# Performance work log

Measured on AMD Instinct MI355X. Metric: run time of the kernel, lower is better.

## Reference

```python
import jax, jax.numpy as jnp
import numpy as np

B, C, H, L, P = 2048, 128, 4, 2, 106
D = C // H
N_PRED = B * P


def _ln(x, g, b, eps=1e-5):
    m = jnp.mean(x, -1, keepdims=True)
    v = jnp.mean((x - m) ** 2, -1, keepdims=True)
    return (x - m) / jnp.sqrt(v + eps) * g + b


def _seg_softmax(a, seg, n):
    mx = jax.lax.stop_gradient(jax.ops.segment_max(a, seg, num_segments=n))
    e = jnp.exp(a - mx[seg])
    den = jax.ops.segment_sum(e, seg, num_segments=n)
    return e / jnp.maximum(den[seg], 1e-16)


def _hgt_layer(xn, xp, edges, kqv_nw, kqv_nb, kqv_pw, kqv_pb, a_rel, m_rel, p_rel,
               out_nw, out_nb, out_pw, out_pb, skip_n, skip_p):
    # PyG HGTConv: per-node-type KQV, per-edge-type relation transforms, grouped
    # softmax over all incoming edges per destination node, scatter-sum aggregation.
    e_np_src, e_np_dst, e_pn_src, e_pn_dst = edges
    nn_, np_ = xn.shape[0], xp.shape[0]
    kqv_n = (xn @ kqv_nw + kqv_nb).reshape(nn_, 3, H, D)
    kqv_p = (xp @ kqv_pw + kqv_pb).reshape(np_, 3, H, D)
    kn, qn, vn = kqv_n[:, 0], kqv_n[:, 1], kqv_n[:, 2]
    kp, qp, vp = kqv_p[:, 0], kqv_p[:, 1], kqv_p[:, 2]
    # relation-specific (per edge type, per head) transforms of all source nodes
    k0 = jnp.einsum('nhd,hde->nhe', kn, a_rel[0])  # news -> predicate
    v0 = jnp.einsum('nhd,hde->nhe', vn, m_rel[0])
    k1 = jnp.einsum('nhd,hde->nhe', kp, a_rel[1])  # predicate -> news
    v1 = jnp.einsum('nhd,hde->nhe', vp, m_rel[1])
    scale = 1.0 / jnp.sqrt(jnp.float32(D))
    a0 = jnp.sum(qp[e_np_dst] * k0[e_np_src], -1) * p_rel[0] * scale  # [E0,H]
    a1 = jnp.sum(qn[e_pn_dst] * k1[e_pn_src], -1) * p_rel[1] * scale  # [E1,H]
    n_tot = nn_ + np_
    dst = jnp.concatenate([e_np_dst + nn_, e_pn_dst])  # global dst ids (news first)
    alpha = _seg_softmax(jnp.concatenate([a0, a1]), dst, n_tot)
    msg = jnp.concatenate([v0[e_np_src], v1[e_pn_src]])  # [E,H,D]
    agg = jax.ops.segment_sum(alpha[..., None] * msg, dst, num_segments=n_tot)
    agg = agg.reshape(n_tot, H * D)
    on = jax.nn.gelu(agg[:nn_], approximate=False) @ out_nw + out_nb
    op = jax.nn.gelu(agg[nn_:], approximate=False) @ out_pw + out_pb
    sn = jax.nn.sigmoid(skip_n)
    sp = jax.nn.sigmoid(skip_p)
    return sn * on + (1.0 - sn) * xn, sp * op + (1.0 - sp) * xp


def setup_inputs():
    ks = iter(jax.random.split(jax.random.key(0), 64))
    rn = lambda shape, s=0.02: jax.random.normal(next(ks), shape, jnp.float32) * s
    i = {}
    i['news_emb'] = jax.random.normal(next(ks), (B, 1024), jnp.float32)
    i['base_embs'] = jax.random.normal(next(ks), (P, 1024), jnp.float32)
    i['ctx_w'] = rn((1024, C)); i['ctx_b'] = jnp.zeros((C,), jnp.float32)
    i['proj_w'] = rn((1024, C)); i['proj_b'] = jnp.zeros((C,), jnp.float32)
    i['fus_w'] = rn((2 * C, C)); i['fus_b'] = jnp.zeros((C,), jnp.float32)
    i['enc_w'] = rn((1024, C)); i['enc_b'] = jnp.zeros((C,), jnp.float32)
    i['enc_g'] = jnp.ones((C,), jnp.float32); i['enc_beta'] = jnp.zeros((C,), jnp.float32)
    for t in ('n', 'p'):
        i['lin_%sw' % t] = rn((C, C)); i['lin_%sb' % t] = jnp.zeros((C,), jnp.float32)
        i['lin_%sg' % t] = jnp.ones((C,), jnp.float32); i['lin_%sbeta' % t] = jnp.zeros((C,), jnp.float32)
        i['kqv_%sw' % t] = rn((L, C, 3 * C)); i['kqv_%sb' % t] = jnp.zeros((L, 3 * C), jnp.float32)
        i['out_%sw' % t] = rn((L, C, C)); i['out_%sb' % t] = jnp.zeros((L, C), jnp.float32)
        i['skip_%s' % t] = jnp.ones((L,), jnp.float32)
        i['ln_%sg' % t] = jnp.ones((L, C), jnp.float32); i['ln_%sbeta' % t] = jnp.zeros((L, C), jnp.float32)
    i['a_rel'] = rn((L, 2, H, D, D), 0.1)
    i['m_rel'] = rn((L, 2, H, D, D), 0.1)
    i['p_rel'] = jnp.ones((L, 2, H), jnp.float32)
    i['cls_w'] = rn((C, 2)); i['cls_b'] = jnp.zeros((2,), jnp.float32)
    # news node b owns predicate nodes [b*P, (b+1)*P)
    i['e_np_src'] = jnp.repeat(jnp.arange(B), P)
    i['e_np_dst'] = jnp.arange(N_PRED)
    i['e_pn_src'] = jnp.arange(N_PRED)
    i['e_pn_dst'] = jnp.repeat(jnp.arange(B), P)
    return i


def reference(news_emb, base_embs, ctx_w, ctx_b, proj_w, proj_b, fus_w, fus_b,
              enc_w, enc_b, enc_g, enc_beta,
              lin_nw, lin_nb, lin_ng, lin_nbeta, lin_pw, lin_pb, lin_pg, lin_pbeta,
              kqv_nw, kqv_nb, kqv_pw, kqv_pb, out_nw, out_nb, out_pw, out_pb,
              skip_n, skip_p, ln_ng, ln_nbeta, ln_pg, ln_pbeta,
              a_rel, m_rel, p_rel, cls_w, cls_b,
              e_np_src, e_np_dst, e_pn_src, e_pn_dst):
    b = news_emb.shape[0]
    # DynamicEmbedding: context-conditioned predicate embeddings [b, P, C]
    news_ctx = news_emb @ ctx_w + ctx_b
    pred_base = base_embs @ proj_w + proj_b
    fused = jnp.concatenate([jnp.broadcast_to(pred_base[None], (b, P, C)),
                             jnp.broadcast_to(news_ctx[:, None], (b, P, C))], -1)
    xp = (fused @ fus_w + fus_b).reshape(b * P, C)
    # news encoder: Linear -> LayerNorm -> ELU
    xn = jax.nn.elu(_ln(news_emb @ enc_w + enc_b, enc_g, enc_beta))
    res_n, res_p = xn, xp
    xn = _ln(xn @ lin_nw + lin_nb, lin_ng, lin_nbeta) + res_n
    xp = _ln(xp @ lin_pw + lin_pb, lin_pg, lin_pbeta) + res_p
    edges = (e_np_src, e_np_dst, e_pn_src, e_pn_dst)
    for l in range(L):
        xn2, xp2 = _hgt_layer(xn, xp, edges, kqv_nw[l], kqv_nb[l], kqv_pw[l], kqv_pb[l],
                              a_rel[l], m_rel[l], p_rel[l],
                              out_nw[l], out_nb[l], out_pw[l], out_pb[l],
                              skip_n[l], skip_p[l])
        xn = jax.nn.elu(_ln(xn2 + res_n, ln_ng[l], ln_nbeta[l]))
        xp = jax.nn.elu(_ln(xp2 + res_p, ln_pg[l], ln_pbeta[l]))
        res_n, res_p = xn, xp
    logits = xn @ cls_w + cls_b
    # attention output is constant by construction in the original module:
    # uniform 1/107 everywhere, row (news -> predicates) overwritten with
    # mean of the dummy uniform per-edge weights = 1/num_edges.
    e0 = e_np_src.shape[0]
    att = jnp.full((b, P + 1, P + 1, H), 1.0 / (P + 1), jnp.float32)
    att = att.at[:, 0, 1:, :].set(1.0 / e0)
    return logits, att
```

## Files before the change

kernel.cpp:

```cpp
#include <hip/hip_runtime.h>
#include <math.h>


#define DEVFN __device__ __forceinline__

typedef float nfloat4 __attribute__((ext_vector_type(4)));

DEVFN void nt_store4(float4* addr, float v){
  nfloat4 val = {v,v,v,v};
  __builtin_nontemporal_store(val, reinterpret_cast<nfloat4*>(addr));
}

DEVFN float wsum(float v){
#pragma unroll
  for (int o=32;o;o>>=1) v += __shfl_xor(v,o);
  return v;
}
DEVFN float wmaxr(float v){
#pragma unroll
  for (int o=32;o;o>>=1) v = fmaxf(v,__shfl_xor(v,o));
  return v;
}
DEVFN float gelu_f(float x){ return 0.5f*x*(1.f+erff(x*0.70710678118654752f)); }
DEVFN float elu_f(float x){ return x>0.f?x:expm1f(x); }
DEVFN float sigm(float x){ return 1.f/(1.f+expf(-x)); }

__global__ __launch_bounds__(512,2) void mega(
  const float* __restrict__ xn_enc_g, const float* __restrict__ Vv_g,
  const float* __restrict__ B1v_g, const float* __restrict__ sb1_g,
  const float* __restrict__ AU, const float* __restrict__ AUT,
  const float* __restrict__ sa1,
  const float* __restrict__ Wcomb, const float* __restrict__ bcomb,
  const float* __restrict__ WvC, const float* __restrict__ bv2,
  const float* __restrict__ Wnv, const float* __restrict__ bnv,
  const float* __restrict__ lin_nw, const float* __restrict__ lin_nb,
  const float* __restrict__ lin_ng, const float* __restrict__ lin_nbeta,
  const float* __restrict__ lin_pg, const float* __restrict__ lin_pbeta,
  const float* __restrict__ ln_pg, const float* __restrict__ ln_pbeta,
  const float* __restrict__ out_nw, const float* __restrict__ out_nb,
  const float* __restrict__ out_pw, const float* __restrict__ out_pb,
  const float* __restrict__ skip_n, const float* __restrict__ skip_p,
  const float* __restrict__ ln_ng, const float* __restrict__ ln_nbeta,
  const float* __restrict__ cls_w, const float* __restrict__ cls_b,
  float* __restrict__ out)
{
  __shared__ __align__(16) float xe[512], x1[512], xA[512], W0s[512], Bv[512], Vvs[512];
  __shared__ __align__(16) float scratch[2048];
  __shared__ __align__(16) float ss[2048];
  __shared__ __align__(16) float rowa[512], rowb[512];
  __shared__ float inv0[512], m1s[512], i1s[512];
  __shared__ __align__(16) float4 PK0[256];
  __shared__ __align__(16) float2 PE[256];
  __shared__ __align__(16) float2 Fa[256];
  __shared__ __align__(16) float4 G0B0[64];
  __shared__ __align__(16) float x4T[512];
  const int tid=threadIdx.x, lane=tid&63, wave=tid>>6, w2=wave>>1, half=wave&1;
  const int bid = blockIdx.x;
  const bool isfill = ((bid%3)==2) && (bid/3 < 253);
  if (isfill){
    float4* att4 = reinterpret_cast<float4*>(out + 4096);
    const long b0 = 24 + (long)(bid/3)*8;
#pragma unroll
    for (int r=0;r<8;r++){
      long base=(b0+r)*11449L;
      for (int i=tid;i<11449;i+=512){
        float v=(i>=1&&i<107)?(1.f/217088.f):(1.f/107.f);
        nt_store4(&att4[base+i], v);
      }
    }
    return;
  }
  int nf = (bid+1)/3; if (nf>253) nf=253;
  const int cid = bid - nf;
  const int bbase=cid*4, b=bbase+w2;
  const float sp0=sigm(skip_p[0]), omsp=1.f-sp0, c1=1.f+omsp;
  xe[tid]=xn_enc_g[(long)bbase*128+tid];
  Bv[tid]=B1v_g[(long)bbase*128+tid];
  Vvs[tid]=Vv_g[(long)bbase*128+tid];
  if (tid<64) G0B0[tid]=make_float4(ln_pg[2*tid],ln_pg[2*tid+1],ln_pbeta[2*tid],ln_pbeta[2*tid+1]);
  __syncthreads();
  if (tid<256){
    int wp=tid>>6, c=tid&63;
    float bx=Bv[wp*128+2*c], by=Bv[wp*128+2*c+1];
    PK0[tid]=make_float4(bx,by,lin_pg[2*c],lin_pg[2*c+1]);
    PE[tid]=make_float2(lin_pbeta[2*c]+Vvs[wp*128+2*c], lin_pbeta[2*c+1]+Vvs[wp*128+2*c+1]);
  }
  {
    const int r=tid>>7, j=tid&127;
    const float4* x4=(const float4*)(xe+r*128);
    float a0=lin_nb[j],a1=0.f,a2=0.f,a3=0.f;
#pragma unroll 4
    for (int i=0;i<32;i++){
      float4 xv=x4[i]; int k=4*i;
      a0+=xv.x*lin_nw[k*128+j]; a1+=xv.y*lin_nw[(k+1)*128+j];
      a2+=xv.z*lin_nw[(k+2)*128+j]; a3+=xv.w*lin_nw[(k+3)*128+j];
    }
    rowa[tid]=(a0+a1)+(a2+a3);
  }
  __syncthreads();
  const float4* AU4=(const float4*)AU;
  const float4* AUT4=(const float4*)AUT;
  const float sb = sb1_g[b];
  const int p = half*64 + lane;
  const bool act = (p<106);
  float iv_reg=0.f;
  if (act){
    float dt0=0.f, dt1=0.f;
#pragma unroll 4
    for (int c=0;c<64;c++){
      float4 au=AUT4[c*128+p];
      float4 pk=PK0[w2*64+c];
      dt0 += au.x*pk.x; dt1 += au.y*pk.y;
    }
    iv_reg = rsqrtf((sa1[p]+2.f*(dt0+dt1)+sb)*(1.f/128.f)+1e-5f);
    inv0[w2*128+p]=iv_reg;
  }
  if (half==0){
    const float* rw=rowa+w2*128;
    float t0=rw[lane], t1=rw[lane+64];
    float m=wsum(t0+t1)*(1.f/128.f);
    float d0=t0-m,d1=t1-m;
    float var=wsum(d0*d0+d1*d1)*(1.f/128.f);
    float inv=rsqrtf(var+1e-5f);
    float v0=d0*inv*lin_ng[lane]   +lin_nbeta[lane]   +xe[w2*128+lane];
    float v1=d1*inv*lin_ng[lane+64]+lin_nbeta[lane+64]+xe[w2*128+lane+64];
    x1[w2*128+lane]=v0; x1[w2*128+lane+64]=v1;
    x4T[lane*4+w2]=v0; x4T[(lane+64)*4+w2]=v1;
  }
  __syncthreads();
  {
    float bval=bcomb[tid];
    float p0=bval,p1=bval,p2=bval,p3=bval, q0=0.f,q1=0.f,q2=0.f,q3=0.f;
    const float4* xv4=(const float4*)x4T;
#pragma unroll 4
    for (int k=0;k<128;k+=2){
      float4 xv=xv4[k];  float w=Wcomb[k*512+tid];
      p0+=xv.x*w; p1+=xv.y*w; p2+=xv.z*w; p3+=xv.w*w;
      float4 xv2=xv4[k+1]; float w2=Wcomb[(k+1)*512+tid];
      q0+=xv2.x*w2; q1+=xv2.y*w2; q2+=xv2.z*w2; q3+=xv2.w*w2;
    }
    int h=tid>>7, cc=tid&127, c=cc>>1, par=cc&1;
    int base = c*8 + (h>>1)*4 + (h&1)*2 + par;
    scratch[base]=p0+q0; scratch[512+base]=p1+q1; scratch[1024+base]=p2+q2; scratch[1536+base]=p3+q3;
  }
  __syncthreads();
  if (act){
    const float iv=iv_reg;
    const float4* qp=(const float4*)(scratch+w2*512);
    float s0=0,s1=0,s2=0,s3=0, u0=0,u1=0,u2=0,u3=0;
#pragma unroll 2
    for (int c=0;c<64;c+=2){
      {
        float4 au=AUT4[c*128+p];
        float4 pk=PK0[w2*64+c];
        float2 e=PE[w2*64+c];
        float4 Qa=qp[c*2], Qb=qp[c*2+1];
        float rx=(au.x+pk.x)*iv*pk.z + e.x + au.z;
        float ry=(au.y+pk.y)*iv*pk.w + e.y + au.w;
        s0+=rx*Qa.x+ry*Qa.y; s1+=rx*Qa.z+ry*Qa.w;
        s2+=rx*Qb.x+ry*Qb.y; s3+=rx*Qb.z+ry*Qb.w;
      }
      {
        int c2=c+1;
        float4 au=AUT4[c2*128+p];
        float4 pk=PK0[w2*64+c2];
        float2 e=PE[w2*64+c2];
        float4 Qa=qp[c2*2], Qb=qp[c2*2+1];
        float rx=(au.x+pk.x)*iv*pk.z + e.x + au.z;
        float ry=(au.y+pk.y)*iv*pk.w + e.y + au.w;
        u0+=rx*Qa.x+ry*Qa.y; u1+=rx*Qa.z+ry*Qa.w;
        u2+=rx*Qb.x+ry*Qb.y; u3+=rx*Qb.z+ry*Qb.w;
      }
    }
    ss[w2*512+  0+p]=s0+u0; ss[w2*512+128+p]=s1+u1;
    ss[w2*512+256+p]=s2+u2; ss[w2*512+384+p]=s3+u3;
  }
  __syncthreads();
#pragma unroll
  for (int k=0;k<2;k++){
    int jj=wave*2+k, jb=jj>>2, jh=jj&3;
    float* row = ss + jb*512 + jh*128;
    float v1=(lane<106)? row[lane] : -1e30f;
    float v2=(lane+64<106)? row[lane+64] : -1e30f;
    float mx=wmaxr(fmaxf(v1,v2));
    float e1=(lane<106)? expf(v1-mx):0.f;
    float e2=(lane+64<106)? expf(v2-mx):0.f;
    float den=wsum(e1+e2);
    float rinv=1.f/den;
    if (lane<106) row[lane]=e1*rinv;
    if (lane+64<106) row[lane+64]=e2*rinv;
  }
  __syncthreads();
  float2 yb0,yb1,yb2,yb3;
  {
    float4 pk=PK0[w2*64+lane];
    float2 e=PE[w2*64+lane];
    float2 y0={0,0},y1={0,0},y2={0,0},y3={0,0};
    const float* al = ss + w2*512;
    const float* ivp = inv0 + w2*128;
    const int pst=half*53, pen=pst+53;
    for (int pp=pst; pp<pen; pp++){
      float4 au=AU4[pp*64+lane];
      float ivv=ivp[pp];
      float rx=(au.x+pk.x)*ivv*pk.z+e.x+au.z;
      float ry=(au.y+pk.y)*ivv*pk.w+e.y+au.w;
      float a0=al[pp],a1=al[128+pp],a2=al[256+pp],a3=al[384+pp];
      y0.x+=a0*rx; y0.y+=a0*ry; y1.x+=a1*rx; y1.y+=a1*ry;
      y2.x+=a2*rx; y2.y+=a2*ry; y3.x+=a3*rx; y3.y+=a3*ry;
    }
    yb0=y0; yb1=y1; yb2=y2; yb3=y3;
    if (half==0){
      float2* Yw=(float2*)(scratch+w2*512);
      Yw[lane]=y0; Yw[64+lane]=y1; Yw[128+lane]=y2; Yw[192+lane]=y3;
    }
  }
  __syncthreads();
  if (half==1){
    float2* Yw=(float2*)(scratch+w2*512);
    float2 t;
    t=Yw[lane];     t.x+=yb0.x; t.y+=yb0.y; Yw[lane]=t;
    t=Yw[64+lane];  t.x+=yb1.x; t.y+=yb1.y; Yw[64+lane]=t;
    t=Yw[128+lane]; t.x+=yb2.x; t.y+=yb2.y; Yw[128+lane]=t;
    t=Yw[192+lane]; t.x+=yb3.x; t.y+=yb3.y; Yw[192+lane]=t;
  }
  __syncthreads();
  float* rowd = ss + 512;
  {
    const int r=tid>>7, j=tid&127, h=j>>5, d=j&31;
    const float4* y4=(const float4*)(scratch + r*512 + h*128);
    const float4* x4=(const float4*)(x1 + r*128);
    const float* Wp = WvC + (h*128)*32 + d;
    float a1a=bv2[j], a1b=0.f, a2a=bnv[j], a2b=0.f;
#pragma unroll 2
    for (int i=0;i<32;i+=2){
      float4 yv=y4[i]; float4 xv=x4[i]; int cc=4*i;
      a1a += yv.x*Wp[cc*32]+yv.y*Wp[(cc+1)*32]+yv.z*Wp[(cc+2)*32]+yv.w*Wp[(cc+3)*32];
      a2a += xv.x*Wnv[cc*128+j]+xv.y*Wnv[(cc+1)*128+j]+xv.z*Wnv[(cc+2)*128+j]+xv.w*Wnv[(cc+3)*128+j];
      float4 yv2=y4[i+1]; float4 xv2=x4[i+1]; int c2=4*i+4;
      a1b += yv2.x*Wp[c2*32]+yv2.y*Wp[(c2+1)*32]+yv2.z*Wp[(c2+2)*32]+yv2.w*Wp[(c2+3)*32];
      a2b += xv2.x*Wnv[c2*128+j]+xv2.y*Wnv[(c2+1)*128+j]+xv2.z*Wnv[(c2+2)*128+j]+xv2.w*Wnv[(c2+3)*128+j];
    }
    rowb[tid]=gelu_f(a1a+a1b); rowd[tid]=gelu_f(a2a+a2b);
  }
  __syncthreads();
  {
    const int r=tid>>7, j=tid&127;
    const float4* xb=(const float4*)(rowb+r*128);
    const float4* xd=(const float4*)(rowd+r*128);
    float a1a=out_nb[j], a1b=0.f, a2a=out_pb[j], a2b=0.f;
#pragma unroll 2
    for (int i=0;i<32;i+=2){
      float4 bv_=xb[i]; float4 dv=xd[i]; int cc=4*i;
      a1a += bv_.x*out_nw[cc*128+j]+bv_.y*out_nw[(cc+1)*128+j]+bv_.z*out_nw[(cc+2)*128+j]+bv_.w*out_nw[(cc+3)*128+j];
      a2a += dv.x*out_pw[cc*128+j]+dv.y*out_pw[(cc+1)*128+j]+dv.z*out_pw[(cc+2)*128+j]+dv.w*out_pw[(cc+3)*128+j];
      float4 bv2_=xb[i+1]; float4 dv2=xd[i+1]; int c2=4*i+4;
      a1b += bv2_.x*out_nw[c2*128+j]+bv2_.y*out_nw[(c2+1)*128+j]+bv2_.z*out_nw[(c2+2)*128+j]+bv2_.w*out_nw[(c2+3)*128+j];
      a2b += dv2.x*out_pw[c2*128+j]+dv2.y*out_pw[(c2+1)*128+j]+dv2.z*out_pw[(c2+2)*128+j]+dv2.w*out_pw[(c2+3)*128+j];
    }
    rowa[tid]=a1a+a1b; W0s[tid]=a2a+a2b;
  }
  __syncthreads();
  if (half==0){
    float sn=sigm(skip_n[0]), os=1.f-sn;
    const float* A=rowa+w2*128; const float* Bx=x1+w2*128; const float* R=xe+w2*128;
    float t0=sn*A[lane]+os*Bx[lane]+R[lane];
    float t1=sn*A[lane+64]+os*Bx[lane+64]+R[lane+64];
    float m=wsum(t0+t1)*(1.f/128.f);
    float d0=t0-m,d1=t1-m;
    float var=wsum(d0*d0+d1*d1)*(1.f/128.f);
    float inv=rsqrtf(var+1e-5f);
    float v0=elu_f(d0*inv*ln_ng[lane]+ln_nbeta[lane]);
    float v1=elu_f(d1*inv*ln_ng[lane+64]+ln_nbeta[lane+64]);
    xA[w2*128+lane]=v0; xA[w2*128+lane+64]=v1;
    x4T[lane*4+w2]=v0; x4T[(lane+64)*4+w2]=v1;
  }
  if (tid<256){
    int wp=tid>>6, c=tid&63;
    Fa[tid]=make_float2(omsp*PE[tid].x + sp0*W0s[wp*128+2*c]   + Vvs[wp*128+2*c],
                        omsp*PE[tid].y + sp0*W0s[wp*128+2*c+1] + Vvs[wp*128+2*c+1]);
  }
  __syncthreads();
  {
    float bval=bcomb[512+tid];
    float p0=bval,p1=bval,p2=bval,p3=bval, q0=0.f,q1=0.f,q2=0.f,q3=0.f;
    const float4* xv4=(const float4*)x4T;
    const float* W=Wcomb+65536;
#pragma unroll 4
    for (int k=0;k<128;k+=2){
      float4 xv=xv4[k];  float w=W[k*512+tid];
      p0+=xv.x*w; p1+=xv.y*w; p2+=xv.z*w; p3+=xv.w*w;
      float4 xv2=xv4[k+1]; float w2=W[(k+1)*512+tid];
      q0+=xv2.x*w2; q1+=xv2.y*w2; q2+=xv2.z*w2; q3+=xv2.w*w2;
    }
    int h=tid>>7, cc=tid&127, c=cc>>1, par=cc&1;
    int base = c*8 + (h>>1)*4 + (h&1)*2 + par;
    scratch[base]=p0+q0; scratch[512+base]=p1+q1; scratch[1024+base]=p2+q2; scratch[1536+base]=p3+q3;
  }
  __syncthreads();
  if (act){
    const float iv=iv_reg;
    float st0=0.f, st1=0.f, sq0=0.f, sq1=0.f;
#pragma unroll 2
    for (int c=0;c<64;c+=2){
      {
        float4 au=AUT4[c*128+p];
        float4 pk=PK0[w2*64+c];
        float2 f=Fa[w2*64+c];
        float t0=omsp*((au.x+pk.x)*iv*pk.z) + f.x + c1*au.z;
        float t1=omsp*((au.y+pk.y)*iv*pk.w) + f.y + c1*au.w;
        st0+=t0+t1; sq0+=t0*t0+t1*t1;
      }
      {
        int c2=c+1;
        float4 au=AUT4[c2*128+p];
        float4 pk=PK0[w2*64+c2];
        float2 f=Fa[w2*64+c2];
        float t0=omsp*((au.x+pk.x)*iv*pk.z) + f.x + c1*au.z;
        float t1=omsp*((au.y+pk.y)*iv*pk.w) + f.y + c1*au.w;
        st1+=t0+t1; sq1+=t0*t0+t1*t1;
      }
    }
    float mA=(st0+st1)*(1.f/128.f);
    float ivA=rsqrtf(fmaxf((sq0+sq1)*(1.f/128.f)-mA*mA,0.f)+1e-5f);
    m1s[w2*128+p]=mA; i1s[w2*128+p]=ivA;
    const float4* qp=(const float4*)(scratch+w2*512);
    float s0=0,s1=0,s2=0,s3=0, u0=0,u1=0,u2=0,u3=0;
#pragma unroll 2
    for (int c=0;c<64;c+=2){
      {
        float4 au=AUT4[c*128+p];
        float4 pk=PK0[w2*64+c];
        float2 f=Fa[w2*64+c];
        float4 gb=G0B0[c];
        float4 Qa=qp[c*2], Qb=qp[c*2+1];
        float t0=omsp*((au.x+pk.x)*iv*pk.z) + f.x + c1*au.z;
        float t1=omsp*((au.y+pk.y)*iv*pk.w) + f.y + c1*au.w;
        float r0=elu_f((t0-mA)*ivA*gb.x+gb.z);
        float r1=elu_f((t1-mA)*ivA*gb.y+gb.w);
        s0+=r0*Qa.x+r1*Qa.y; s1+=r0*Qa.z+r1*Qa.w;
        s2+=r0*Qb.x+r1*Qb.y; s3+=r0*Qb.z+r1*Qb.w;
      }
      {
        int c2=c+1;
        float4 au=AUT4[c2*128+p];
        float4 pk=PK0[w2*64+c2];
        float2 f=Fa[w2*64+c2];
        float4 gb=G0B0[c2];
        float4 Qa=qp[c2*2], Qb=qp[c2*2+1];
        float t0=omsp*((au.x+pk.x)*iv*pk.z) + f.x + c1*au.z;
        float t1=omsp*((au.y+pk.y)*iv*pk.w) + f.y + c1*au.w;
        float r0=elu_f((t0-mA)*ivA*gb.x+gb.z);
        float r1=elu_f((t1-mA)*ivA*gb.y+gb.w);
        u0+=r0*Qa.x+r1*Qa.y; u1+=r0*Qa.z+r1*Qa.w;
        u2+=r0*Qb.x+r1*Qb.y; u3+=r0*Qb.z+r1*Qb.w;
      }
    }
    ss[w2*512+  0+p]=s0+u0; ss[w2*512+128+p]=s1+u1;
    ss[w2*512+256+p]=s2+u2; ss[w2*512+384+p]=s3+u3;
  }
  __syncthreads();
#pragma unroll
  for (int k=0;k<2;k++){
    int jj=wave*2+k, jb=jj>>2, jh=jj&3;
    float* row = ss + jb*512 + jh*128;
    float v1=(lane<106)? row[lane] : -1e30f;
    float v2=(lane+64<106)? row[lane+64] : -1e30f;
    float mx=wmaxr(fmaxf(v1,v2));
    float e1=(lane<106)? expf(v1-mx):0.f;
    float e2=(lane+64<106)? expf(v2-mx):0.f;
    float den=wsum(e1+e2);
    float rinv=1.f/den;
    if (lane<106) row[lane]=e1*rinv;
    if (lane+64<106) row[lane+64]=e2*rinv;
  }
  __syncthreads();
  {
    float4 pk=PK0[w2*64+lane];
    float2 f=Fa[w2*64+lane];
    float4 gb=G0B0[lane];
    float2 y0={0,0},y1={0,0},y2={0,0},y3={0,0};
    const float* al = ss + w2*512;
    const float* ivp = inv0 + w2*128;
    const float* mp = m1s + w2*128;
    const float* ip = i1s + w2*128;
    const int pst=half*53, pen=pst+53;
    for (int pp=pst; pp<pen; pp++){
      float4 au=AU4[pp*64+lane];
      float ivv=ivp[pp], m=mp[pp], i2=ip[pp];
      float tx=omsp*((au.x+pk.x)*ivv*pk.z) + f.x + c1*au.z;
      float ty=omsp*((au.y+pk.y)*ivv*pk.w) + f.y + c1*au.w;
      float r0=elu_f((tx-m)*i2*gb.x+gb.z);
      float r1=elu_f((ty-m)*i2*gb.y+gb.w);
      float a0=al[pp],a1=al[128+pp],a2=al[256+pp],a3=al[384+pp];
      y0.x+=a0*r0; y0.y+=a0*r1; y1.x+=a1*r0; y1.y+=a1*r1;
      y2.x+=a2*r0; y2.y+=a2*r1; y3.x+=a3*r0; y3.y+=a3*r1;
    }
    yb0=y0; yb1=y1; yb2=y2; yb3=y3;
    if (half==0){
      float2* Yw=(float2*)(scratch+w2*512);
      Yw[lane]=y0; Yw[64+lane]=y1; Yw[128+lane]=y2; Yw[192+lane]=y3;
    }
  }
  __syncthreads();
  if (half==1){
    float2* Yw=(float2*)(scratch+w2*512);
    float2 t;
    t=Yw[lane];     t.x+=yb0.x; t.y+=yb0.y; Yw[lane]=t;
    t=Yw[64+lane];  t.x+=yb1.x; t.y+=yb1.y; Yw[64+lane]=t;
    t=Yw[128+lane]; t.x+=yb2.x; t.y+=yb2.y; Yw[128+lane]=t;
    t=Yw[192+lane]; t.x+=yb3.x; t.y+=yb3.y; Yw[192+lane]=t;
  }
  __syncthreads();
  {
    const int r=tid>>7, j=tid&127, h=j>>5, d=j&31;
    const float4* y4=(const float4*)(scratch + r*512 + h*128);
    const float* Wp = WvC + 16384 + (h*128)*32 + d;
    float aa=bv2[128+j], ab=0.f;
#pragma unroll 2
    for (int i=0;i<32;i+=2){
      float4 yv=y4[i]; int cc=4*i;
      aa += yv.x*Wp[cc*32]+yv.y*Wp[(cc+1)*32]+yv.z*Wp[(cc+2)*32]+yv.w*Wp[(cc+3)*32];
      float4 yv2=y4[i+1]; int c2=4*i+4;
      ab += yv2.x*Wp[c2*32]+yv2.y*Wp[(c2+1)*32]+yv2.z*Wp[(c2+2)*32]+yv2.w*Wp[(c2+3)*32];
    }
    rowb[tid]=gelu_f(aa+ab);
  }
  __syncthreads();
  {
    const int r=tid>>7, j=tid&127;
    const float4* xb=(const float4*)(rowb+r*128);
    const float* W=out_nw+16384;
    float aa=out_nb[128+j], ab=0.f;
#pragma unroll 2
    for (int i=0;i<32;i+=2){
      float4 bv_=xb[i]; int cc=4*i;
      aa += bv_.x*W[cc*128+j]+bv_.y*W[(cc+1)*128+j]+bv_.z*W[(cc+2)*128+j]+bv_.w*W[(cc+3)*128+j];
      float4 bv2_=xb[i+1]; int c2=4*i+4;
      ab += bv2_.x*W[c2*128+j]+bv2_.y*W[(c2+1)*128+j]+bv2_.z*W[(c2+2)*128+j]+bv2_.w*W[(c2+3)*128+j];
    }
    rowa[tid]=aa+ab;
  }
  __syncthreads();
  if (half==0){
    float sn=sigm(skip_n[1]), os=1.f-sn;
    const float* A=rowa+w2*128; const float* Bx=xA+w2*128;
    float t0=sn*A[lane]+os*Bx[lane]+Bx[lane];
    float t1=sn*A[lane+64]+os*Bx[lane+64]+Bx[lane+64];
    float m=wsum(t0+t1)*(1.f/128.f);
    float d0=t0-m,d1=t1-m;
    float var=wsum(d0*d0+d1*d1)*(1.f/128.f);
    float inv=rsqrtf(var+1e-5f);
    float xv0=elu_f(d0*inv*ln_ng[128+lane]+ln_nbeta[128+lane]);
    float xv1=elu_f(d1*inv*ln_ng[128+lane+64]+ln_nbeta[128+lane+64]);
    float a0=xv0*cls_w[lane*2]  +xv1*cls_w[(lane+64)*2];
    float a1=xv0*cls_w[lane*2+1]+xv1*cls_w[(lane+64)*2+1];
    a0=wsum(a0); a1=wsum(a1);
    if (lane==0){ out[b*2]=a0+cls_b[0]; out[b*2+1]=a1+cls_b[1]; }
  }
}

__global__ __launch_bounds__(256) void prep(
  const float* __restrict__ news_emb,
  const float* __restrict__ ctx_w, const float* __restrict__ ctx_b,
  const float* __restrict__ enc_w, const float* __restrict__ enc_b,
  const float* __restrict__ enc_g, const float* __restrict__ enc_beta,
  const float* __restrict__ proj_w, const float* __restrict__ proj_b,
  const float* __restrict__ base_embs,
  const float* __restrict__ fus_w, const float* __restrict__ fus_b,
  const float* __restrict__ lin_pw, const float* __restrict__ lin_pb,
  const float* __restrict__ kqv_nw, const float* __restrict__ kqv_nb,
  const float* __restrict__ kqv_pw, const float* __restrict__ kqv_pb,
  const float* __restrict__ a_rel, const float* __restrict__ m_rel,
  const float* __restrict__ p_rel,
  float* __restrict__ Wcomb, float* __restrict__ bcomb,
  float* __restrict__ WvC, float* __restrict__ bv2,
  float* __restrict__ Wnv, float* __restrict__ bnv,
  float* __restrict__ AU, float* __restrict__ AUT, float* __restrict__ sa1,
  float* __restrict__ xn_enc, float* __restrict__ Vv,
  float* __restrict__ B1v, float* __restrict__ sb1)
{
  __shared__ __align__(16) float pool[6400];
  const int blk=blockIdx.x, tid=threadIdx.x, lane=tid&63, wid=tid>>6;
  if (blk < 135){
    float* sh  = pool;
    float* row1= pool+2048;
    float* row2= pool+2176;
    float* row3= pool+2304;
    float* red = pool+2432;
    if (blk < 16){
      int l=blk>>3, jq=blk&7, h=jq>>1, cc0=(jq&1)*64;
      float* wk = sh;
      float ps = p_rel[(l*2+1)*4+h]*0.17677669529663687f;
      for (int idx=tid; idx<2048; idx+=256){
        int e=idx>>6, cl=idx&63;
        float acc=0.f;
#pragma unroll
        for (int d=0;d<32;d++)
          acc += kqv_pw[(long)l*49152 + (cc0+cl)*384 + h*32 + d]
               * a_rel[((l*2+1)*4+h)*1024 + d*32 + e];
        wk[e*64+cl]=acc*ps;
      }
      __syncthreads();
      for (int idx=tid; idx<8192; idx+=256){
        int c=idx>>6, jl=idx&63;
        float acc=0.f;
#pragma unroll
        for (int e=0;e<32;e++) acc += kqv_nw[(long)l*49152 + c*384 + 128 + h*32 + e]*wk[e*64+jl];
        Wcomb[(long)l*65536 + c*512 + h*128 + cc0 + jl]=acc;
      }
      if (tid<64){
        float acc=0.f;
#pragma unroll
        for (int e=0;e<32;e++) acc += kqv_nb[l*384 + 128 + h*32 + e]*wk[e*64+tid];
        bcomb[l*512 + h*128 + cc0 + tid]=acc;
      }
    } else if (blk < 24){
      int t=blk-16, l=t>>2, h=t&3;
      float* rl = sh;
      for (int i=tid;i<1024;i+=256) rl[i]=m_rel[((l*2+1)*4+h)*1024+i];
      __syncthreads();
      for (int idx=tid; idx<4096; idx+=256){
        int cc=idx>>5, d=idx&31;
        float acc=0.f;
#pragma unroll
        for (int dp=0;dp<32;dp++) acc += kqv_pw[(long)l*49152 + cc*384 + 256 + h*32 + dp]*rl[dp*32+d];
        WvC[l*16384 + (h*128+cc)*32 + d]=acc;
      }
    } else if (blk==24){
      {
        int l=tid>>7, j=tid&127, h=(j>>5)&3, d=j&31;
        float acc=0.f;
#pragma unroll
        for (int dp=0;dp<32;dp++) acc += kqv_pb[l*384+256+h*32+dp]*m_rel[((l*2+1)*4+h)*1024+dp*32+d];
        bv2[l*128+j]=acc;
      }
      if (tid < 128){
        int j=tid, h=j>>5, d=j&31;
        float acc=0.f;
#pragma unroll
        for (int dp=0;dp<32;dp++) acc += kqv_nb[256+h*32+dp]*m_rel[h*1024+dp*32+d];
        bnv[j]=acc;
      }
    } else if (blk < 29){
      int h=blk-25;
      float* rl=sh;
      for (int i=tid;i<1024;i+=256) rl[i]=m_rel[h*1024+i];
      __syncthreads();
      for (int idx=tid; idx<4096; idx+=256){
        int c=idx>>5, d=idx&31;
        float acc=0.f;
#pragma unroll
        for (int dp=0;dp<32;dp++) acc += kqv_nw[c*384+256+h*32+dp]*rl[dp*32+d];
        Wnv[c*128 + h*32 + d]=acc;
      }
    } else {
      int p = blk-29;
      float* xs1=pool;
      int j=tid&127, kg=tid>>7;
      for (int i=tid;i<1024;i+=256) xs1[i]=base_embs[(long)p*1024+i];
      __syncthreads();
      float acc=0.f;
#pragma unroll 4
      for (int k=0;k<512;k++) acc += xs1[kg*512+k]*proj_w[(long)(kg*512+k)*128+j];
      red[tid]=acc; __syncthreads();
      if (tid<128) row1[tid]=red[tid]+red[tid+128]+proj_b[tid];
      __syncthreads();
      acc=0.f;
#pragma unroll 4
      for (int i=0;i<64;i++) acc += row1[kg*64+i]*fus_w[(long)(kg*64+i)*128+j];
      red[tid]=acc; __syncthreads();
      if (tid<128) row2[tid]=red[tid]+red[tid+128]+fus_b[tid];
      __syncthreads();
      acc=0.f;
#pragma unroll 4
      for (int i=0;i<64;i++) acc += row2[kg*64+i]*lin_pw[(long)(kg*64+i)*128+j];
      red[tid]=acc; __syncthreads();
      if (tid<128) row3[tid]=red[tid]+red[tid+128];
      __syncthreads();
      if (wid==0){
        float t0=row3[lane], t1=row3[lane+64];
        float m=wsum(t0+t1)*(1.f/128.f);
        t0-=m; t1-=m;
        float ssq=wsum(t0*t0+t1*t1);
        row3[lane]=t0; row3[lane+64]=t1;
        if (lane==0) sa1[p]=ssq;
      }
      __syncthreads();
      if (tid<64){
        float4 v = make_float4(row3[2*tid],row3[2*tid+1],row2[2*tid],row2[2*tid+1]);
        ((float4*)AU)[p*64+tid]=v;
        ((float4*)AUT)[tid*128+p]=v;
      }
    }
  } else {
    float* xs   = pool;
    float* redL = pool+4096;
    float* rowsC= pool+5120;
    float* Vraw = pool+5632;
    float* bVbL = pool+6144;
    float* bB1L = pool+6272;
    const int r0=(blk-135)*4;
    const int j=tid&127, kg=tid>>7;
    for (int r=0;r<4;r++){
      float4 v=*(const float4*)(news_emb+(long)(r0+r)*1024+tid*4);
      *(float4*)(&xs[r*1024+tid*4])=v;
    }
    {
      float acc=0.f;
#pragma unroll 4
      for (int i=0;i<64;i++) acc += ctx_b[kg*64+i]*fus_w[(128+kg*64+i)*128+j];
      redL[tid]=acc; __syncthreads();
      if (tid<128) bVbL[tid]=redL[tid]+redL[128+tid];
      __syncthreads();
      acc=0.f;
#pragma unroll 4
      for (int i=0;i<64;i++) acc += bVbL[kg*64+i]*lin_pw[(kg*64+i)*128+j];
      redL[tid]=acc; __syncthreads();
      if (tid<128) bB1L[tid]=redL[tid]+redL[128+tid]+lin_pb[tid];
      __syncthreads();
    }
    float ae0=0,ae1=0,ae2=0,ae3=0, ac0=0,ac1=0,ac2=0,ac3=0;
    {
      const float* We=enc_w+(long)(kg*512)*128+j;
      const float* Wc=ctx_w+(long)(kg*512)*128+j;
#pragma unroll 2
      for (int k=0;k<512;k++){
        float we=We[(long)k*128], wc=Wc[(long)k*128];
        float v0=xs[kg*512+k], v1=xs[1024+kg*512+k], v2=xs[2048+kg*512+k], v3=xs[3072+kg*512+k];
        ae0+=v0*we; ae1+=v1*we; ae2+=v2*we; ae3+=v3*we;
        ac0+=v0*wc; ac1+=v1*wc; ac2+=v2*wc; ac3+=v3*wc;
      }
    }
    redL[tid]=ae0; redL[256+tid]=ae1; redL[512+tid]=ae2; redL[768+tid]=ae3;
    __syncthreads();
    {
      float t0=redL[wid*256+lane]+redL[wid*256+128+lane]+enc_b[lane];
      float t1=redL[wid*256+lane+64]+redL[wid*256+128+lane+64]+enc_b[lane+64];
      float m=wsum(t0+t1)*(1.f/128.f);
      float d0=t0-m,d1=t1-m;
      float var=wsum(d0*d0+d1*d1)*(1.f/128.f);
      float inv=rsqrtf(var+1e-5f);
      xn_enc[(long)(r0+wid)*128+lane]   =elu_f(d0*inv*enc_g[lane]   +enc_beta[lane]);
      xn_enc[(long)(r0+wid)*128+lane+64]=elu_f(d1*inv*enc_g[lane+64]+enc_beta[lane+64]);
    }
    __syncthreads();
    redL[tid]=ac0; redL[256+tid]=ac1; redL[512+tid]=ac2; redL[768+tid]=ac3;
    __syncthreads();
    for (int i=tid;i<512;i+=256){
      int r=i>>7,jj=i&127;
      rowsC[r*128+jj]=redL[r*256+jj]+redL[r*256+128+jj];
    }
    __syncthreads();
    {
      const float* Wf=fus_w+(128+kg*64)*128+j;
      float a0=0,a1=0,a2=0,a3=0;
#pragma unroll 4
      for (int i=0;i<64;i++){
        float wv=Wf[i*128];
        a0+=rowsC[kg*64+i]*wv; a1+=rowsC[128+kg*64+i]*wv;
        a2+=rowsC[256+kg*64+i]*wv; a3+=rowsC[384+kg*64+i]*wv;
      }
      redL[tid]=a0; redL[256+tid]=a1; redL[512+tid]=a2; redL[768+tid]=a3;
    }
    __syncthreads();
    for (int i=tid;i<512;i+=256){
      int r=i>>7,jj=i&127;
      float v=redL[r*256+jj]+redL[r*256+128+jj];
      Vraw[r*128+jj]=v;
      Vv[(long)(r0+r)*128+jj]=v+bVbL[jj];
    }
    __syncthreads();
    {
      const float* Wl=lin_pw+(kg*64)*128+j;
      float a0=0,a1=0,a2=0,a3=0;
#pragma unroll 4
      for (int i=0;i<64;i++){
        float wv=Wl[i*128];
        a0+=Vraw[kg*64+i]*wv; a1+=Vraw[128+kg*64+i]*wv;
        a2+=Vraw[256+kg*64+i]*wv; a3+=Vraw[384+kg*64+i]*wv;
      }
      redL[tid]=a0; redL[256+tid]=a1; redL[512+tid]=a2; redL[768+tid]=a3;
    }
    __syncthreads();
    {
      float t0=redL[wid*256+lane]+redL[wid*256+128+lane]+bB1L[lane];
      float t1=redL[wid*256+lane+64]+redL[wid*256+128+lane+64]+bB1L[lane+64];
      float m=wsum(t0+t1)*(1.f/128.f);
      t0-=m; t1-=m;
      float ssq=wsum(t0*t0+t1*t1);
      B1v[(long)(r0+wid)*128+lane]=t0;
      B1v[(long)(r0+wid)*128+lane+64]=t1;
      if (lane==0) sb1[r0+wid]=ssq;
    }
  }
}

__global__ __launch_bounds__(256) void fill_att2(float4* __restrict__ att4){
  const float v1 = 1.f/107.f, v2 = 1.f/217088.f;
  long base = (long)blockIdx.x*11449;
  for (int i=threadIdx.x; i<11449; i+=256){
    float v = (i>=1 && i<107) ? v2 : v1;
    nt_store4(&att4[base+i], v);
  }
}

extern "C" void kernel_launch(void* const* d_in, const int* in_sizes, int n_in,
                              void* d_out, int out_size, void* d_ws, size_t ws_size,
                              hipStream_t stream) {
  const float* news_emb = (const float*)d_in[0];
  const float* base_embs= (const float*)d_in[1];
  const float* ctx_w  = (const float*)d_in[2];
  const float* ctx_b  = (const float*)d_in[3];
  const float* proj_w = (const float*)d_in[4];
  const float* proj_b = (const float*)d_in[5];
  const float* fus_w  = (const float*)d_in[6];
  const float* fus_b  = (const float*)d_in[7];
  const float* enc_w  = (const float*)d_in[8];
  const float* enc_b  = (const float*)d_in[9];
  const float* enc_g  = (const float*)d_in[10];
  const float* enc_beta=(const float*)d_in[11];
  const float* lin_nw = (const float*)d_in[12];
  const float* lin_nb = (const float*)d_in[13];
  const float* lin_ng = (const float*)d_in[14];
  const float* lin_nbeta=(const float*)d_in[15];
  const float* kqv_nw = (const float*)d_in[16];
  const float* kqv_nb = (const float*)d_in[17];
  const float* out_nw = (const float*)d_in[18];
  const float* out_nb = (const float*)d_in[19];
  const float* skip_n = (const float*)d_in[20];
  const float* ln_ng  = (const float*)d_in[21];
  const float* ln_nbeta=(const float*)d_in[22];
  const float* lin_pw = (const float*)d_in[23];
  const float* lin_pb = (const float*)d_in[24];
  const float* lin_pg = (const float*)d_in[25];
  const float* lin_pbeta=(const float*)d_in[26];
  const float* kqv_pw = (const float*)d_in[27];
  const float* kqv_pb = (const float*)d_in[28];
  const float* out_pw = (const float*)d_in[29];
  const float* out_pb = (const float*)d_in[30];
  const float* skip_p = (const float*)d_in[31];
  const float* ln_pg  = (const float*)d_in[32];
  const float* ln_pbeta=(const float*)d_in[33];
  const float* a_rel  = (const float*)d_in[34];
  const float* m_rel  = (const float*)d_in[35];
  const float* p_rel  = (const float*)d_in[36];
  const float* cls_w  = (const float*)d_in[37];
  const float* cls_b  = (const float*)d_in[38];
  (void)in_sizes; (void)n_in; (void)out_size; (void)d_ws; (void)ws_size;

  float* out = (float*)d_out;
  float* S = out + 4096;
  float* xn_enc = S + 0;
  float* Vv     = S + 262144;
  float* B1v    = S + 524288;
  float* sb1    = S + 786432;
  float* sa1    = S + 788480;
  float* AU     = S + 788608;
  float* AUT    = S + 815744;
  float* WvC    = S + 848512;
  float* bv2    = S + 881280;
  float* Wnv    = S + 881536;
  float* bnv    = S + 897920;
  float* Wcomb  = S + 898048;
  float* bcomb  = S + 1029120;

  dim3 blk(256), blkL(512);
  prep<<<647,blk,0,stream>>>(news_emb,ctx_w,ctx_b,enc_w,enc_b,enc_g,enc_beta,
      proj_w,proj_b,base_embs,fus_w,fus_b,lin_pw,lin_pb,
      kqv_nw,kqv_nb,kqv_pw,kqv_pb,a_rel,m_rel,p_rel,
      Wcomb,bcomb,WvC,bv2,Wnv,bnv,AU,AUT,sa1,xn_enc,Vv,B1v,sb1);
  mega<<<765,blkL,0,stream>>>(xn_enc,Vv,B1v,sb1,AU,AUT,sa1,Wcomb,bcomb,WvC,bv2,Wnv,bnv,
      lin_nw,lin_nb,lin_ng,lin_nbeta,lin_pg,lin_pbeta,ln_pg,ln_pbeta,
      out_nw,out_nb,out_pw,out_pb,skip_n,skip_p,ln_ng,ln_nbeta,cls_w,cls_b,out);
  fill_att2<<<24,blk,0,stream>>>(reinterpret_cast<float4*>(S));
}
```

Before: 313.3 us.

## Halve mega block size to two batch items per 256-thread block

Changes the fused kernel from 512-thread blocks handling four samples each to 256-thread blocks handling two, doubling the compute block count. Fill blocks are no longer interleaved every third block; they all come first. The combined-weight matmuls are rewritten so each thread computes two output columns for two rows, and shared memory arrays are halved. The aim is more resident blocks and finer-grained scheduling, at the cost of reloading weights in twice as many blocks.

```diff
diff --git a/kernel.cpp b/kernel.cpp
--- a/kernel.cpp
+++ b/kernel.cpp
@@ -25,7 +25,7 @@
 DEVFN float elu_f(float x){ return x>0.f?x:expm1f(x); }
 DEVFN float sigm(float x){ return 1.f/(1.f+expf(-x)); }
 
-__global__ __launch_bounds__(512,2) void mega(
+__global__ __launch_bounds__(256,2) void mega(
   const float* __restrict__ xn_enc_g, const float* __restrict__ Vv_g,
   const float* __restrict__ B1v_g, const float* __restrict__ sb1_g,
   const float* __restrict__ AU, const float* __restrict__ AUT,
@@ -44,45 +44,42 @@
   const float* __restrict__ cls_w, const float* __restrict__ cls_b,
   float* __restrict__ out)
 {
-  __shared__ __align__(16) float xe[512], x1[512], xA[512], W0s[512], Bv[512], Vvs[512];
-  __shared__ __align__(16) float scratch[2048];
-  __shared__ __align__(16) float ss[2048];
-  __shared__ __align__(16) float rowa[512], rowb[512];
-  __shared__ float inv0[512], m1s[512], i1s[512];
-  __shared__ __align__(16) float4 PK0[256];
-  __shared__ __align__(16) float2 PE[256];
-  __shared__ __align__(16) float2 Fa[256];
+  __shared__ __align__(16) float xe[256], x1[256], xA[256], W0s[256], Bv[256], Vvs[256];
+  __shared__ __align__(16) float scratch[1024];
+  __shared__ __align__(16) float ss[1024];
+  __shared__ __align__(16) float rowa[256], rowb[256];
+  __shared__ float inv0[256], m1s[256], i1s[256];
+  __shared__ __align__(16) float4 PK0[128];
+  __shared__ __align__(16) float2 PE[128];
+  __shared__ __align__(16) float2 Fa[128];
   __shared__ __align__(16) float4 G0B0[64];
-  __shared__ __align__(16) float x4T[512];
+  __shared__ __align__(16) float x2T[256];
   const int tid=threadIdx.x, lane=tid&63, wave=tid>>6, w2=wave>>1, half=wave&1;
   const int bid = blockIdx.x;
-  const bool isfill = ((bid%3)==2) && (bid/3 < 253);
-  if (isfill){
+  if (bid < 253){
     float4* att4 = reinterpret_cast<float4*>(out + 4096);
-    const long b0 = 24 + (long)(bid/3)*8;
+    const long b0 = 24 + (long)bid*8;
 #pragma unroll
     for (int r=0;r<8;r++){
       long base=(b0+r)*11449L;
-      for (int i=tid;i<11449;i+=512){
+      for (int i=tid;i<11449;i+=256){
         float v=(i>=1&&i<107)?(1.f/217088.f):(1.f/107.f);
         nt_store4(&att4[base+i], v);
       }
     }
     return;
   }
-  int nf = (bid+1)/3; if (nf>253) nf=253;
-  const int cid = bid - nf;
-  const int bbase=cid*4, b=bbase+w2;
+  const int cid = bid - 253;
+  const int bbase=cid*2, b=bbase+w2;
   const float sp0=sigm(skip_p[0]), omsp=1.f-sp0, c1=1.f+omsp;
   xe[tid]=xn_enc_g[(long)bbase*128+tid];
   Bv[tid]=B1v_g[(long)bbase*128+tid];
   Vvs[tid]=Vv_g[(long)bbase*128+tid];
   if (tid<64) G0B0[tid]=make_float4(ln_pg[2*tid],ln_pg[2*tid+1],ln_pbeta[2*tid],ln_pbeta[2*tid+1]);
   __syncthreads();
-  if (tid<256){
+  if (tid<128){
     int wp=tid>>6, c=tid&63;
-    float bx=Bv[wp*128+2*c], by=Bv[wp*128+2*c+1];
-    PK0[tid]=make_float4(bx,by,lin_pg[2*c],lin_pg[2*c+1]);
+    PK0[tid]=make_float4(Bv[wp*128+2*c],Bv[wp*128+2*c+1],lin_pg[2*c],lin_pg[2*c+1]);
     PE[tid]=make_float2(lin_pbeta[2*c]+Vvs[wp*128+2*c], lin_pbeta[2*c+1]+Vvs[wp*128+2*c+1]);
   }
   {
@@ -125,23 +122,30 @@
     float v0=d0*inv*lin_ng[lane]   +lin_nbeta[lane]   +xe[w2*128+lane];
     float v1=d1*inv*lin_ng[lane+64]+lin_nbeta[lane+64]+xe[w2*128+lane+64];
     x1[w2*128+lane]=v0; x1[w2*128+lane+64]=v1;
-    x4T[lane*4+w2]=v0; x4T[(lane+64)*4+w2]=v1;
-  }
-  __syncthreads();
-  {
-    float bval=bcomb[tid];
-    float p0=bval,p1=bval,p2=bval,p3=bval, q0=0.f,q1=0.f,q2=0.f,q3=0.f;
-    const float4* xv4=(const float4*)x4T;
+    x2T[lane*2+w2]=v0; x2T[(lane+64)*2+w2]=v1;
+  }
+  __syncthreads();
+  {
+    float b0v=bcomb[tid], b1v=bcomb[256+tid];
+    float a00=b0v,a01=b1v,a10=0.f,a11=0.f, c00=0.f,c01=0.f,c10=0.f,c11=0.f;
+    const float2* xv2=(const float2*)x2T;
 #pragma unroll 4
     for (int k=0;k<128;k+=2){
-      float4 xv=xv4[k];  float w=Wcomb[k*512+tid];
-      p0+=xv.x*w; p1+=xv.y*w; p2+=xv.z*w; p3+=xv.w*w;
-      float4 xv2=xv4[k+1]; float w2=Wcomb[(k+1)*512+tid];
-      q0+=xv2.x*w2; q1+=xv2.y*w2; q2+=xv2.z*w2; q3+=xv2.w*w2;
-    }
-    int h=tid>>7, cc=tid&127, c=cc>>1, par=cc&1;
-    int base = c*8 + (h>>1)*4 + (h&1)*2 + par;
-    scratch[base]=p0+q0; scratch[512+base]=p1+q1; scratch[1024+base]=p2+q2; scratch[1536+base]=p3+q3;
+      float2 xv=xv2[k];  float w0=Wcomb[k*512+tid], w1=Wcomb[k*512+256+tid];
+      a00+=xv.x*w0; a01+=xv.x*w1; a10+=xv.y*w0; a11+=xv.y*w1;
+      float2 xw=xv2[k+1]; float u0=Wcomb[(k+1)*512+tid], u1=Wcomb[(k+1)*512+256+tid];
+      c00+=xw.x*u0; c01+=xw.x*u1; c10+=xw.y*u0; c11+=xw.y*u1;
+    }
+    {
+      int j=tid, h=j>>7, cc=j&127, c=cc>>1, par=cc&1;
+      int base=c*8+(h>>1)*4+(h&1)*2+par;
+      scratch[base]=a00+c00; scratch[512+base]=a10+c10;
+    }
+    {
+      int j=tid+256, h=j>>7, cc=j&127, c=cc>>1, par=cc&1;
+      int base=c*8+(h>>1)*4+(h&1)*2+par;
+      scratch[base]=a01+c01; scratch[512+base]=a11+c11;
+    }
   }
   __syncthreads();
   if (act){
@@ -224,7 +228,7 @@
     t=Yw[192+lane]; t.x+=yb3.x; t.y+=yb3.y; Yw[192+lane]=t;
   }
   __syncthreads();
-  float* rowd = ss + 512;
+  float* rowd = ss;
   {
     const int r=tid>>7, j=tid&127, h=j>>5, d=j&31;
     const float4* y4=(const float4*)(scratch + r*512 + h*128);
@@ -272,29 +276,36 @@
     float v0=elu_f(d0*inv*ln_ng[lane]+ln_nbeta[lane]);
     float v1=elu_f(d1*inv*ln_ng[lane+64]+ln_nbeta[lane+64]);
     xA[w2*128+lane]=v0; xA[w2*128+lane+64]=v1;
-    x4T[lane*4+w2]=v0; x4T[(lane+64)*4+w2]=v1;
-  }
-  if (tid<256){
+    x2T[lane*2+w2]=v0; x2T[(lane+64)*2+w2]=v1;
+  }
+  if (tid<128){
     int wp=tid>>6, c=tid&63;
     Fa[tid]=make_float2(omsp*PE[tid].x + sp0*W0s[wp*128+2*c]   + Vvs[wp*128+2*c],
                         omsp*PE[tid].y + sp0*W0s[wp*128+2*c+1] + Vvs[wp*128+2*c+1]);
   }
   __syncthreads();
   {
-    float bval=bcomb[512+tid];
-    float p0=bval,p1=bval,p2=bval,p3=bval, q0=0.f,q1=0.f,q2=0.f,q3=0.f;
-    const float4* xv4=(const float4*)x4T;
     const float* W=Wcomb+65536;
+    float b0v=bcomb[512+tid], b1v=bcomb[512+256+tid];
+    float a00=b0v,a01=b1v,a10=0.f,a11=0.f, c00=0.f,c01=0.f,c10=0.f,c11=0.f;
+    const float2* xv2=(const float2*)x2T;
 #pragma unroll 4
     for (int k=0;k<128;k+=2){
-      float4 xv=xv4[k];  float w=W[k*512+tid];
-      p0+=xv.x*w; p1+=xv.y*w; p2+=xv.z*w; p3+=xv.w*w;
-      float4 xv2=xv4[k+1]; float w2=W[(k+1)*512+tid];
-      q0+=xv2.x*w2; q1+=xv2.y*w2; q2+=xv2.z*w2; q3+=xv2.w*w2;
-    }
-    int h=tid>>7, cc=tid&127, c=cc>>1, par=cc&1;
-    int base = c*8 + (h>>1)*4 + (h&1)*2 + par;
-    scratch[base]=p0+q0; scratch[512+base]=p1+q1; scratch[1024+base]=p2+q2; scratch[1536+base]=p3+q3;
+      float2 xv=xv2[k];  float w0=W[k*512+tid], w1=W[k*512+256+tid];
+      a00+=xv.x*w0; a01+=xv.x*w1; a10+=xv.y*w0; a11+=xv.y*w1;
+      float2 xw=xv2[k+1]; float u0=W[(k+1)*512+tid], u1=W[(k+1)*512+256+tid];
+      c00+=xw.x*u0; c01+=xw.x*u1; c10+=xw.y*u0; c11+=xw.y*u1;
+    }
+    {
+      int j=tid, h=j>>7, cc=j&127, c=cc>>1, par=cc&1;
+      int base=c*8+(h>>1)*4+(h&1)*2+par;
+      scratch[base]=a00+c00; scratch[512+base]=a10+c10;
+    }
+    {
+      int j=tid+256, h=j>>7, cc=j&127, c=cc>>1, par=cc&1;
+      int base=c*8+(h>>1)*4+(h&1)*2+par;
+      scratch[base]=a01+c01; scratch[512+base]=a11+c11;
+    }
   }
   __syncthreads();
   if (act){
@@ -764,12 +775,12 @@
   float* Wcomb  = S + 898048;
   float* bcomb  = S + 1029120;
 
-  dim3 blk(256), blkL(512);
+  dim3 blk(256);
   prep<<<647,blk,0,stream>>>(news_emb,ctx_w,ctx_b,enc_w,enc_b,enc_g,enc_beta,
       proj_w,proj_b,base_embs,fus_w,fus_b,lin_pw,lin_pb,
       kqv_nw,kqv_nb,kqv_pw,kqv_pb,a_rel,m_rel,p_rel,
       Wcomb,bcomb,WvC,bv2,Wnv,bnv,AU,AUT,sa1,xn_enc,Vv,B1v,sb1);
-  mega<<<765,blkL,0,stream>>>(xn_enc,Vv,B1v,sb1,AU,AUT,sa1,Wcomb,bcomb,WvC,bv2,Wnv,bnv,
+  mega<<<1277,blk,0,stream>>>(xn_enc,Vv,B1v,sb1,AU,AUT,sa1,Wcomb,bcomb,WvC,bv2,Wnv,bnv,
       lin_nw,lin_nb,lin_ng,lin_nbeta,lin_pg,lin_pbeta,ln_pg,ln_pbeta,
       out_nw,out_nb,out_pw,out_pb,skip_n,skip_p,ln_ng,ln_nbeta,cls_w,cls_b,out);
   fill_att2<<<24,blk,0,stream>>>(reinterpret_cast<float4*>(S));
```

Result: slower. 349.6 us (+11.6%).
